# Performance work log

Measured on AMD Instinct MI355X. Metric: run time of the kernel, lower is better.

The kernel has to match this reference:

```python
import jax, jax.numpy as jnp
import numpy as np

B, S, D, H, DFF = 2, 2048, 1024, 16, 4096
DK = D // H
EPS = 1e-6


def layer_norm(x, alpha, bias):
    # torch: alpha * (x - mean) / (std_unbiased + eps) + bias
    mean = jnp.mean(x, axis=-1, keepdims=True)
    std = jnp.sqrt(jnp.var(x, axis=-1, keepdims=True, ddof=1))
    return alpha * (x - mean) / (std + EPS) + bias


def setup_inputs() -> dict:
    key = jax.random.key(0)
    ks = jax.random.split(key, 10)
    w = lambda k, shape: (jax.random.normal(k, shape, jnp.float32) * 0.02)
    return {
        "x": jax.random.normal(ks[0], (B, S, D), jnp.float32),
        "mask": jnp.ones((B, 1, 1, S), jnp.int32),
        "wq": w(ks[1], (D, D)),
        "wk": w(ks[2], (D, D)),
        "wv": w(ks[3], (D, D)),
        "wo": w(ks[4], (D, D)),
        "w1": w(ks[5], (DFF, D)),
        "b1": jnp.zeros((DFF,), jnp.float32),
        "w2": w(ks[6], (D, DFF)),
        "b2": jnp.zeros((D,), jnp.float32),
        "alpha1": jnp.ones((D,), jnp.float32),
        "bias1": jnp.zeros((D,), jnp.float32),
        "alpha2": jnp.ones((D,), jnp.float32),
        "bias2": jnp.zeros((D,), jnp.float32),
    }


def reference(x, mask, wq, wk, wv, wo, w1, b1, w2, b2, alpha1, bias1, alpha2, bias2):
    # --- residual 1: pre-norm + self-attention ---
    xn = layer_norm(x, alpha1, bias1)                      # [B,S,D]
    q = (xn @ wq.T).reshape(B, S, H, DK).transpose(0, 2, 1, 3)  # [B,H,S,DK]
    k = (xn @ wk.T).reshape(B, S, H, DK).transpose(0, 2, 1, 3)
    v = (xn @ wv.T).reshape(B, S, H, DK).transpose(0, 2, 1, 3)
    scores = jnp.einsum("bhqd,bhkd->bhqk", q, k) / jnp.sqrt(jnp.float32(DK))
    scores = jnp.where(mask == 0, jnp.float32(-1e9), scores)
    attn = jax.nn.softmax(scores, axis=-1)                 # [B,H,S,S]
    av = jnp.einsum("bhqk,bhkd->bhqd", attn, v)            # [B,H,S,DK]
    av = av.transpose(0, 2, 1, 3).reshape(B, S, D)
    x = x + av @ wo.T                                      # dropout p=0
    # --- residual 2: pre-norm + FFN ---
    xn2 = layer_norm(x, alpha2, bias2)
    h = jax.nn.relu(xn2 @ w1.T + b1)                       # [B,S,DFF]
    x = x + h @ w2.T + b2
    return x
```

## Files before the change

### kernel.cpp

```cpp
#include <hip/hip_runtime.h>

#define B_   2
#define S_   2048
#define D_   1024
#define H_   16
#define DK_  64
#define DFF_ 4096
#define NTOK (B_ * S_)

#define QSCALE 0.18033688011112042f

typedef __bf16 bf16x8 __attribute__((ext_vector_type(8)));
typedef __bf16 bf16x4 __attribute__((ext_vector_type(4)));
typedef float  f32x4  __attribute__((ext_vector_type(4)));

#if __has_builtin(__builtin_amdgcn_exp2f)
#define EXP2(x) __builtin_amdgcn_exp2f(x)
#else
#define EXP2(x) exp2f(x)
#endif

__device__ __forceinline__ void ld16(const __bf16* g, __bf16* l) {
  __builtin_amdgcn_global_load_lds(
      (const __attribute__((address_space(1))) void*)g,
      (__attribute__((address_space(3))) void*)l, 16, 0, 0);
}

#define RAW_BAR()     __asm__ __volatile__("s_barrier" ::: "memory")
#define SCHED_FENCE() __builtin_amdgcn_sched_barrier(0)

__device__ __forceinline__ void xcd_swz256(int& bx, int& by) {
  const int gx = gridDim.x;
  const int flat = blockIdx.y * gx + blockIdx.x;
  const int x = flat & 7, n = flat >> 3;
  if (gx == 16) { by = ((x >> 1) << 2) + (n >> 3); bx = ((x & 1) << 3) + (n & 7); }
  else          { by = (x << 1) + (n >> 2);        bx = n & 3; }
}

__device__ __forceinline__ void lda4(bf16x8 (&afr)[4], const __bf16* hb,
                                     int abase, int f0) {
#pragma unroll
  for (int i = 0; i < 4; ++i)
    afr[i] = *(const bf16x8*)(hb + abase + (f0 + i) * 512);
}

__device__ __forceinline__ void ldb4(bf16x8 (&bfr)[4], const __bf16* hb,
                                     int bbase) {
#pragma unroll
  for (int j = 0; j < 4; ++j)
    bfr[j] = *(const bf16x8*)(hb + bbase + j * 512);
}

__device__ __forceinline__ void mm16(f32x4 (&acc)[8][4], const bf16x8 (&afr)[4],
                                     const bf16x8 (&bfr)[4], int r0) {
#pragma unroll
  for (int i = 0; i < 4; ++i)
#pragma unroll
    for (int j = 0; j < 4; ++j)
      acc[r0 + i][j] =
          __builtin_amdgcn_mfma_f32_16x16x32_bf16(afr[i], bfr[j], acc[r0 + i][j], 0, 0, 0);
}

__device__ __forceinline__ void gemm_core_256(
    const __bf16* __restrict__ A, const __bf16* __restrict__ W,
    int ld, int kLen, int rowA0, int rowW0,
    f32x4 (&acc)[8][4], __bf16* Ls)
{
  const int t = threadIdx.x;
  const int lane = t & 63, wv = t >> 6;
  const int wm = wv >> 2, wn = wv & 3;
  const int l15 = lane & 15, q4 = lane >> 4;

  const int lane_rd = l15 * 32 + ((q4 * 8) ^ (((l15 >> 1) & 3) << 3));
  const int abase = wm * 4096 + lane_rd;
  const int bbase = wn * 2048 + lane_rd;

  const int sc0 = t ^ ((t >> 3) & 3);
  const __bf16* gA0 = A + (size_t)(rowA0 + (sc0 >> 2)) * ld + (sc0 & 3) * 8;
  const __bf16* gA1 = gA0 + (size_t)128 * ld;
  const __bf16* gW0 = W + (size_t)(rowW0 + (sc0 >> 2)) * ld + (sc0 & 3) * 8;
  const __bf16* gW1 = gW0 + (size_t)128 * ld;
  const int d0 = wv * 512, d1 = 4096 + wv * 512;

#pragma unroll
  for (int i = 0; i < 8; ++i)
#pragma unroll
    for (int j = 0; j < 4; ++j) acc[i][j] = (f32x4){0.f, 0.f, 0.f, 0.f};

#define HBASE(slot, mat, h) (Ls + ((((slot)*2) + (mat)) * 2 + (h)) * 8192)
#define STG_A(tt, h, slot) do { __bf16* _d = HBASE(slot, 0, h);              \
    const int _ko = (tt) * 64 + (h) * 32;                                    \
    ld16(gA0 + _ko, _d + d0); ld16(gA1 + _ko, _d + d1); } while (0)
#define STG_B(tt, h, slot) do { __bf16* _d = HBASE(slot, 1, h);              \
    const int _ko = (tt) * 64 + (h) * 32;                                    \
    ld16(gW0 + _ko, _d + d0); ld16(gW1 + _ko, _d + d1); } while (0)
#define MFMA_PH(r0) do { RAW_BAR(); SCHED_FENCE();                           \
    __builtin_amdgcn_s_setprio(1); mm16(acc, afr, bfr, r0);                  \
    __builtin_amdgcn_s_setprio(0); SCHED_FENCE(); RAW_BAR(); } while (0)

  const int NT = kLen >> 6;
  bf16x8 afr[4], bfr[4];

  STG_A(0, 0, 0); STG_A(0, 1, 0); STG_B(0, 0, 0); STG_B(0, 1, 0);
  STG_B(1, 0, 1); STG_A(1, 0, 1); STG_B(1, 1, 1);
  __asm__ __volatile__("s_waitcnt vmcnt(6)" ::: "memory");
  RAW_BAR(); SCHED_FENCE();

  for (int u = 0; u < NT; u += 2) {
    const bool g2 = (u + 2) < NT, g3 = (u + 3) < NT;
    lda4(afr, HBASE(0, 0, 0), abase, 0); ldb4(bfr, HBASE(0, 1, 0), bbase);
    STG_A(u + 1, 1, 1);
    MFMA_PH(0);
    lda4(afr, HBASE(0, 0, 0), abase, 4);
    if (g2) STG_B(u + 2, 0, 0);
    MFMA_PH(4);
    lda4(afr, HBASE(0, 0, 1), abase, 0); ldb4(bfr, HBASE(0, 1, 1), bbase);
    if (g2) STG_A(u + 2, 0, 0);
    MFMA_PH(0);
    lda4(afr, HBASE(0, 0, 1), abase, 4);
    if (g2) {
      STG_B(u + 2, 1, 0);
      __asm__ __volatile__("s_waitcnt vmcnt(6)" ::: "memory");
    } else {
      __asm__ __volatile__("s_waitcnt vmcnt(0)" ::: "memory");
    }
    MFMA_PH(4);
    lda4(afr, HBASE(1, 0, 0), abase, 0); ldb4(bfr, HBASE(1, 1, 0), bbase);
    if (g2) STG_A(u + 2, 1, 0);
    MFMA_PH(0);
    lda4(afr, HBASE(1, 0, 0), abase, 4);
    if (g3) STG_B(u + 3, 0, 1);
    MFMA_PH(4);
    lda4(afr, HBASE(1, 0, 1), abase, 0); ldb4(bfr, HBASE(1, 1, 1), bbase);
    if (g3) STG_A(u + 3, 0, 1);
    MFMA_PH(0);
    lda4(afr, HBASE(1, 0, 1), abase, 4);
    if (g3) STG_B(u + 3, 1, 1);
    __asm__ __volatile__("s_waitcnt vmcnt(6)" ::: "memory");
    MFMA_PH(4);
  }
#undef HBASE
#undef STG_A
#undef STG_B
#undef MFMA_PH
}

__global__ __launch_bounds__(512, 2) void gemm_qkv_256(
    const __bf16* __restrict__ xn,
    const __bf16* __restrict__ wqb, const __bf16* __restrict__ wkb,
    const __bf16* __restrict__ wvb,
    __bf16* __restrict__ qo, __bf16* __restrict__ ko, __bf16* __restrict__ vto)
{
  __shared__ __align__(16) __bf16 Ls[65536];
  int bx, by; xcd_swz256(bx, by);
  const __bf16* W = blockIdx.z == 0 ? wqb : (blockIdx.z == 1 ? wkb : wvb);
  f32x4 acc[8][4];
  gemm_core_256(xn, W, D_, D_, by * 256, bx * 256, acc, Ls);

  const int t = threadIdx.x, lane = t & 63, wv = t >> 6;
  const int wm = wv >> 2, wn = wv & 3;
  const int l15 = lane & 15, q4 = lane >> 4;
  const int row0 = by * 256 + wm * 128;
  const int col0 = bx * 256 + wn * 64;

  if (blockIdx.z < 2) {
    __bf16* o = blockIdx.z == 0 ? qo : ko;
    const float sc = blockIdx.z == 0 ? QSCALE : 1.0f;
#pragma unroll
    for (int fr = 0; fr < 8; ++fr)
#pragma unroll
      for (int fc = 0; fc < 4; ++fc) {
        const int col = col0 + fc * 16 + l15;
#pragma unroll
        for (int r = 0; r < 4; ++r) {
          const int row = row0 + fr * 16 + q4 * 4 + r;
          o[(size_t)row * D_ + col] = (__bf16)(acc[fr][fc][r] * sc);
        }
      }
  } else {
#pragma unroll
    for (int fr = 0; fr < 8; ++fr)
#pragma unroll
      for (int fc = 0; fc < 4; ++fc) {
        const int tok0 = row0 + fr * 16 + q4 * 4;
        const int c    = col0 + fc * 16 + l15;
        const int b0 = tok0 >> 11, s0 = tok0 & (S_ - 1);
        const int hh = c >> 6, dd = c & (DK_ - 1);
        bf16x4 pk;
#pragma unroll
        for (int r = 0; r < 4; ++r) pk[r] = (__bf16)acc[fr][fc][r];
        *(bf16x4*)&vto[(size_t)((b0 * H_ + hh) * DK_ + dd) * S_ + s0] = pk;
      }
  }
}

__global__ __launch_bounds__(512, 2) void gemm_ffn1_256(
    const __bf16* __restrict__ A, const __bf16* __restrict__ W,
    __bf16* __restrict__ outb, const float* __restrict__ bias)
{
  __shared__ __align__(16) __bf16 Ls[65536];
  int bx, by; xcd_swz256(bx, by);
  f32x4 acc[8][4];
  gemm_core_256(A, W, D_, D_, by * 256, bx * 256, acc, Ls);

  const int t = threadIdx.x, lane = t & 63, wv = t >> 6;
  const int wm = wv >> 2, wn = wv & 3;
  const int l15 = lane & 15, q4 = lane >> 4;
  const int row0 = by * 256 + wm * 128;
  const int col0 = bx * 256 + wn * 64;

#pragma unroll
  for (int fr = 0; fr < 8; ++fr)
#pragma unroll
    for (int fc = 0; fc < 4; ++fc) {
      const int col = col0 + fc * 16 + l15;
      const float bs = bias[col];
#pragma unroll
      for (int r = 0; r < 4; ++r) {
        const int row = row0 + fr * 16 + q4 * 4 + r;
        outb[(size_t)row * DFF_ + col] = (__bf16)fmaxf(acc[fr][fc][r] + bs, 0.0f);
      }
    }
}

__global__ __launch_bounds__(512, 2) void gemm_ffn2_sk4(
    const __bf16* __restrict__ A, const __bf16* __restrict__ W,
    __bf16* __restrict__ pp)
{
  __shared__ __align__(16) __bf16 Ls[65536];
  int bx, by; xcd_swz256(bx, by);
  const int z = blockIdx.z;
  f32x4 acc[8][4];
  gemm_core_256(A + (size_t)z * 1024, W + (size_t)z * 1024, DFF_, 1024,
                by * 256, bx * 256, acc, Ls);

  const int t = threadIdx.x, lane = t & 63, wv = t >> 6;
  const int wm = wv >> 2, wn = wv & 3;
  const int l15 = lane & 15, q4 = lane >> 4;
  const int row0 = by * 256 + wm * 128;
  const int col0 = bx * 256 + wn * 64;
  __bf16* out = pp + (size_t)z * NTOK * D_;

#pragma unroll
  for (int fr = 0; fr < 8; ++fr)
#pragma unroll
    for (int fc = 0; fc < 4; ++fc) {
      const int col = col0 + fc * 16 + l15;
#pragma unroll
      for (int r = 0; r < 4; ++r) {
        const int row = row0 + fr * 16 + q4 * 4 + r;
        out[(size_t)row * D_ + col] = (__bf16)acc[fr][fc][r];
      }
    }
}

__global__ __launch_bounds__(512, 2) void gemm_oproj_256(
    const __bf16* __restrict__ A, const __bf16* __restrict__ W,
    float* __restrict__ p0, float* __restrict__ p1)
{
  __shared__ __align__(16) __bf16 Ls[65536];
  int bx, by; xcd_swz256(bx, by);
  const int z = blockIdx.z;
  f32x4 acc[8][4];
  gemm_core_256(A + (size_t)z * 512, W + (size_t)z * 512, D_, 512,
                by * 256, bx * 256, acc, Ls);

  const int t = threadIdx.x, lane = t & 63, wv = t >> 6;
  const int wm = wv >> 2, wn = wv & 3;
  const int l15 = lane & 15, q4 = lane >> 4;
  const int row0 = by * 256 + wm * 128;
  const int col0 = bx * 256 + wn * 64;
  float* out = z == 0 ? p0 : p1;

#pragma unroll
  for (int fr = 0; fr < 8; ++fr)
#pragma unroll
    for (int fc = 0; fc < 4; ++fc) {
      const int col = col0 + fc * 16 + l15;
#pragma unroll
      for (int r = 0; r < 4; ++r) {
        const int row = row0 + fr * 16 + q4 * 4 + r;
        out[(size_t)row * D_ + col] = acc[fr][fc][r];
      }
    }
}

__global__ __launch_bounds__(256) void oproj_ln_reduce(
    const float* __restrict__ x, const float* __restrict__ p0,
    const float* __restrict__ p1, const float* __restrict__ alpha,
    const float* __restrict__ bias, float* __restrict__ x1,
    __bf16* __restrict__ xn2)
{
  const int row = blockIdx.x;
  const int t = threadIdx.x;
  const size_t base = (size_t)row * D_;
  float4 v  = ((const float4*)(x  + base))[t];
  const float4 a0 = ((const float4*)(p0 + base))[t];
  const float4 a1 = ((const float4*)(p1 + base))[t];
  v.x += a0.x + a1.x; v.y += a0.y + a1.y;
  v.z += a0.z + a1.z; v.w += a0.w + a1.w;
  ((float4*)(x1 + base))[t] = v;

  float s  = v.x + v.y + v.z + v.w;
  float ss = v.x * v.x + v.y * v.y + v.z * v.z + v.w * v.w;
#pragma unroll
  for (int m = 1; m < 64; m <<= 1) {
    s  += __shfl_xor(s, m);
    ss += __shfl_xor(ss, m);
  }
  __shared__ float red[8];
  if ((t & 63) == 0) { red[t >> 6] = s; red[4 + (t >> 6)] = ss; }
  __syncthreads();
  s  = red[0] + red[1] + red[2] + red[3];
  ss = red[4] + red[5] + red[6] + red[7];
  const float mean = s * (1.0f / D_);
  float var = (ss - (float)D_ * mean * mean) * (1.0f / (D_ - 1));
  var = fmaxf(var, 0.0f);
  const float inv = 1.0f / (sqrtf(var) + 1e-6f);
  const float4 al = ((const float4*)alpha)[t];
  const float4 bi = ((const float4*)bias)[t];
  bf16x4 o;
  o.x = (__bf16)(al.x * (v.x - mean) * inv + bi.x);
  o.y = (__bf16)(al.y * (v.y - mean) * inv + bi.y);
  o.z = (__bf16)(al.z * (v.z - mean) * inv + bi.z);
  o.w = (__bf16)(al.w * (v.w - mean) * inv + bi.w);
  ((bf16x4*)(xn2 + base))[t] = o;
}

__global__ __launch_bounds__(256) void ffn2_reduce(
    const float* __restrict__ x1, const __bf16* __restrict__ pp,
    const float* __restrict__ b2, float* __restrict__ out)
{
  const int idx4 = blockIdx.x * 256 + threadIdx.x;
  float4 v = ((const float4*)x1)[idx4];
  const float4 bs = ((const float4*)b2)[idx4 & 255];
  const size_t st = (size_t)NTOK * D_ / 4;
  const bf16x4 q0 = ((const bf16x4*)pp)[idx4];
  const bf16x4 q1 = ((const bf16x4*)pp)[idx4 + st];
  const bf16x4 q2 = ((const bf16x4*)pp)[idx4 + 2 * st];
  const bf16x4 q3 = ((const bf16x4*)pp)[idx4 + 3 * st];
  v.x += bs.x + (float)q0[0] + (float)q1[0] + (float)q2[0] + (float)q3[0];
  v.y += bs.y + (float)q0[1] + (float)q1[1] + (float)q2[1] + (float)q3[1];
  v.z += bs.z + (float)q0[2] + (float)q1[2] + (float)q2[2] + (float)q3[2];
  v.w += bs.w + (float)q0[3] + (float)q1[3] + (float)q2[3] + (float)q3[3];
  ((float4*)out)[idx4] = v;
}

struct CastJobs {
  const float* src[6];
  __bf16* dst[6];
  int n4[6];
};

__global__ __launch_bounds__(256) void cast_ln_kernel(
    CastJobs cj, const float* __restrict__ x, const float* __restrict__ alpha,
    const float* __restrict__ bias, __bf16* __restrict__ xn1)
{
  const int j = blockIdx.y;
  if (j < 6) {
    const int i = blockIdx.x * 256 + threadIdx.x;
    if (i < cj.n4[j]) {
      float4 v = ((const float4*)cj.src[j])[i];
      bf16x4 o;
      o.x = (__bf16)v.x; o.y = (__bf16)v.y; o.z = (__bf16)v.z; o.w = (__bf16)v.w;
      ((bf16x4*)cj.dst[j])[i] = o;
    }
    return;
  }
  const int row = blockIdx.x;
  const int t = threadIdx.x;
  const float4 v = ((const float4*)(x + (size_t)row * D_))[t];
  float s  = v.x + v.y + v.z + v.w;
  float ss = v.x * v.x + v.y * v.y + v.z * v.z + v.w * v.w;
#pragma unroll
  for (int m = 1; m < 64; m <<= 1) {
    s  += __shfl_xor(s, m);
    ss += __shfl_xor(ss, m);
  }
  __shared__ float red[8];
  if ((t & 63) == 0) { red[t >> 6] = s; red[4 + (t >> 6)] = ss; }
  __syncthreads();
  s  = red[0] + red[1] + red[2] + red[3];
  ss = red[4] + red[5] + red[6] + red[7];
  const float mean = s * (1.0f / D_);
  float var = (ss - (float)D_ * mean * mean) * (1.0f / (D_ - 1));
  var = fmaxf(var, 0.0f);
  const float inv = 1.0f / (sqrtf(var) + 1e-6f);
  const float4 al = ((const float4*)alpha)[t];
  const float4 bi = ((const float4*)bias)[t];
  bf16x4 o;
  o.x = (__bf16)(al.x * (v.x - mean) * inv + bi.x);
  o.y = (__bf16)(al.y * (v.y - mean) * inv + bi.y);
  o.z = (__bf16)(al.z * (v.z - mean) * inv + bi.z);
  o.w = (__bf16)(al.w * (v.w - mean) * inv + bi.w);
  ((bf16x4*)(xn1 + (size_t)row * D_))[t] = o;
}

__global__ __launch_bounds__(256) void attn_kernel(
    const __bf16* __restrict__ qg, const __bf16* __restrict__ kg,
    const __bf16* __restrict__ vtg, const int* __restrict__ mask,
    __bf16* __restrict__ av)
{
  __shared__ __align__(16) __bf16 Ks[2][64 * 64];
  __shared__ __align__(16) __bf16 Vt[2][64 * 64];
  __shared__ __align__(16) __bf16 Ps[128 * 72];
  __shared__ int Dd[32];

  const int t = threadIdx.x, lane = t & 63, wv = t >> 6;
  const int l15 = lane & 15, q4 = lane >> 4;
  const int bh = blockIdx.x;
  const int b = bh >> 4, h = bh & (H_ - 1);
  const int q0 = blockIdx.y * 128;

  const int srow = lane & 7, sc8 = lane >> 3;
  const __bf16* qg0 = qg + (size_t)(b * S_ + q0 + 32 * wv + srow) * D_ + h * DK_ + sc8 * 8;
  __bf16* lQ = Ps + wv * 2304;
#pragma unroll
  for (int p = 0; p < 4; ++p)
    ld16(qg0 + (size_t)(8 * p) * D_, lQ + 512 * p);

  const __bf16* kg0 = kg + (size_t)(b * S_ + 16 * wv + srow) * D_ + h * DK_ + sc8 * 8;
  const __bf16* vt0 = vtg + (size_t)(bh * DK_ + 16 * wv + srow) * S_ + sc8 * 8;

  if (t < 32) Dd[t] = 0;

  ld16(kg0,                  Ks[0] + wv * 1024);
  ld16(kg0 + (size_t)8 * D_, Ks[0] + wv * 1024 + 512);
  ld16(vt0,                  Vt[0] + wv * 1024);
  ld16(vt0 + (size_t)8 * S_, Vt[0] + wv * 1024 + 512);

  __syncthreads();

  {
    const int4* m4 = (const int4*)(mask + (size_t)b * S_) + t * 2;
    const int4 a = m4[0], c = m4[1];
    const bool anyz = (a.x == 0) | (a.y == 0) | (a.z == 0) | (a.w == 0) |
                      (c.x == 0) | (c.y == 0) | (c.z == 0) | (c.w == 0);
    if (anyz) Dd[t >> 3] = 1;
  }
  __syncthreads();
  const bool blockDirty = (__ballot(Dd[lane & 31] != 0) != 0ull);

  const int fb = ((l15 >> 3) << 9) + (q4 << 6) + ((l15 & 7) << 3);
  const int mrow = b * S_;

  bf16x8 bq[2][2];
#pragma unroll
  for (int j = 0; j < 2; ++j)
#pragma unroll
    for (int s = 0; s < 2; ++s)
      bq[j][s] = *(const bf16x8*)(lQ + j * 1024 + s * 256 + fb);

  bf16x8 bones;
#pragma unroll
  for (int e = 0; e < 8; ++e) bones[e] = (__bf16)1.0f;

  f32x4 lacc[2];
  f32x4 oacc[2][4];
#pragma unroll
  for (int m = 0; m < 2; ++m) {
    lacc[m] = (f32x4){0.f, 0.f, 0.f, 0.f};
#pragma unroll
    for (int jd = 0; jd < 4; ++jd) oacc[m][jd] = (f32x4){0.f, 0.f, 0.f, 0.f};
  }

  for (int kv0 = 0; kv0 < S_; kv0 += 64) {
    const int buf = (kv0 >> 6) & 1;
    if (kv0 + 64 < S_) {
      const size_t nk = (size_t)(kv0 + 64);
      ld16(kg0 + nk * D_,              Ks[buf ^ 1] + wv * 1024);
      ld16(kg0 + (nk + 8) * D_,        Ks[buf ^ 1] + wv * 1024 + 512);
      ld16(vt0 + nk,                   Vt[buf ^ 1] + wv * 1024);
      ld16(vt0 + (size_t)8 * S_ + nk,  Vt[buf ^ 1] + wv * 1024 + 512);
    }

    f32x4 sacc[4][2];
#pragma unroll
    for (int i = 0; i < 4; ++i)
#pragma unroll
      for (int j = 0; j < 2; ++j) sacc[i][j] = (f32x4){0.f, 0.f, 0.f, 0.f};
    __builtin_amdgcn_s_setprio(1);
#pragma unroll
    for (int i = 0; i < 4; ++i)
#pragma unroll
      for (int s = 0; s < 2; ++s) {
        bf16x8 ak = *(const bf16x8*)(Ks[buf] + i * 1024 + fb + s * 256);
#pragma unroll
        for (int j = 0; j < 2; ++j)
          sacc[i][j] = __builtin_amdgcn_mfma_f32_16x16x32_bf16(ak, bq[j][s], sacc[i][j], 0, 0, 0);
      }
    __builtin_amdgcn_s_setprio(0);

    if (blockDirty && Dd[kv0 >> 6]) {
#pragma unroll
      for (int i = 0; i < 4; ++i)
#pragma unroll
        for (int r = 0; r < 4; ++r)
          if (mask[mrow + kv0 + 16 * i + 4 * q4 + r] == 0) {
            sacc[i][0][r] = -1e30f;
            sacc[i][1][r] = -1e30f;
          }
    }

#pragma unroll
    for (int j = 0; j < 2; ++j)
#pragma unroll
      for (int i = 0; i < 4; ++i) {
        bf16x4 pb;
#pragma unroll
        for (int r = 0; r < 4; ++r) pb[r] = (__bf16)EXP2(sacc[i][j][r]);
        *(bf16x4*)(Ps + (wv * 32 + j * 16 + l15) * 72 + 16 * i + q4 * 4) = pb;
      }

    bf16x8 ap[2][2];
#pragma unroll
    for (int m = 0; m < 2; ++m)
#pragma unroll
      for (int s = 0; s < 2; ++s)
        ap[m][s] = *(const bf16x8*)(Ps + (wv * 32 + 16 * m + l15) * 72 + s * 32 + q4 * 8);
    __builtin_amdgcn_s_setprio(1);
#pragma unroll
    for (int jd = 0; jd < 4; ++jd)
#pragma unroll
      for (int s = 0; s < 2; ++s) {
        bf16x8 bv = *(const bf16x8*)(Vt[buf] + jd * 1024 + fb + s * 256);
#pragma unroll
        for (int m = 0; m < 2; ++m)
          oacc[m][jd] = __builtin_amdgcn_mfma_f32_16x16x32_bf16(ap[m][s], bv, oacc[m][jd], 0, 0, 0);
      }
#pragma unroll
    for (int m = 0; m < 2; ++m)
#pragma unroll
      for (int s = 0; s < 2; ++s)
        lacc[m] = __builtin_amdgcn_mfma_f32_16x16x32_bf16(ap[m][s], bones, lacc[m], 0, 0, 0);
    __builtin_amdgcn_s_setprio(0);

    __syncthreads();
  }

#pragma unroll
  for (int m = 0; m < 2; ++m) {
    f32x4 lt;
#pragma unroll
    for (int r = 0; r < 4; ++r) lt[r] = 1.0f / lacc[m][r];
#pragma unroll
    for (int jd = 0; jd < 4; ++jd)
#pragma unroll
      for (int r = 0; r < 4; ++r) {
        int tok = b * S_ + q0 + wv * 32 + 16 * m + q4 * 4 + r;
        int c   = h * DK_ + jd * 16 + l15;
        av[(size_t)tok * D_ + c] = (__bf16)(oacc[m][jd][r] * lt[r]);
      }
  }
}

extern "C" void kernel_launch(void* const* d_in, const int* in_sizes, int n_in,
                              void* d_out, int out_size, void* d_ws, size_t ws_size,
                              hipStream_t stream) {
  const float* x      = (const float*)d_in[0];
  const int*   mask   = (const int*)d_in[1];
  const float* wq     = (const float*)d_in[2];
  const float* wk     = (const float*)d_in[3];
  const float* wv     = (const float*)d_in[4];
  const float* wo     = (const float*)d_in[5];
  const float* w1     = (const float*)d_in[6];
  const float* b1     = (const float*)d_in[7];
  const float* w2     = (const float*)d_in[8];
  const float* b2     = (const float*)d_in[9];
  const float* alpha1 = (const float*)d_in[10];
  const float* bias1  = (const float*)d_in[11];
  const float* alpha2 = (const float*)d_in[12];
  const float* bias2  = (const float*)d_in[13];

  char* ws = (char*)d_ws;
  __bf16* wqb = (__bf16*)(ws + ((size_t)0 << 20));
  __bf16* wkb = (__bf16*)(ws + ((size_t)2 << 20));
  __bf16* wvb = (__bf16*)(ws + ((size_t)4 << 20));
  __bf16* wob = (__bf16*)(ws + ((size_t)6 << 20));
  __bf16* w1b = (__bf16*)(ws + ((size_t)8 << 20));
  __bf16* w2b = (__bf16*)(ws + ((size_t)16 << 20));
  __bf16* xn1 = (__bf16*)(ws + ((size_t)24 << 20));
  __bf16* qb  = (__bf16*)(ws + ((size_t)32 << 20));
  __bf16* kb  = (__bf16*)(ws + ((size_t)40 << 20));
  __bf16* vtb = (__bf16*)(ws + ((size_t)48 << 20));
  __bf16* avb = (__bf16*)(ws + ((size_t)56 << 20));
  float*  x1  = (float*) (ws + ((size_t)64 << 20));
  __bf16* xn2 = (__bf16*)(ws + ((size_t)56 << 20));
  __bf16* hb  = (__bf16*)(ws + ((size_t)24 << 20));
  float*  op0 = (float*) (ws + ((size_t)24 << 20));
  float*  op1 = (float*) (ws + ((size_t)40 << 20));
  __bf16* fpp = (__bf16*)(ws + ((size_t)32 << 20));

  CastJobs cj;
  cj.src[0] = wq; cj.dst[0] = wqb; cj.n4[0] = D_ * D_ / 4;
  cj.src[1] = wk; cj.dst[1] = wkb; cj.n4[1] = D_ * D_ / 4;
  cj.src[2] = wv; cj.dst[2] = wvb; cj.n4[2] = D_ * D_ / 4;
  cj.src[3] = wo; cj.dst[3] = wob; cj.n4[3] = D_ * D_ / 4;
  cj.src[4] = w1; cj.dst[4] = w1b; cj.n4[4] = DFF_ * D_ / 4;
  cj.src[5] = w2; cj.dst[5] = w2b; cj.n4[5] = DFF_ * D_ / 4;

  cast_ln_kernel<<<dim3(DFF_ * D_ / 4 / 256, 7), 256, 0, stream>>>(
      cj, x, alpha1, bias1, xn1);

  gemm_qkv_256<<<dim3(D_ / 256, NTOK / 256, 3), 512, 0, stream>>>(
      xn1, wqb, wkb, wvb, qb, kb, vtb);

  attn_kernel<<<dim3(B_ * H_, S_ / 128), 256, 0, stream>>>(qb, kb, vtb, mask, avb);

  gemm_oproj_256<<<dim3(D_ / 256, NTOK / 256, 2), 512, 0, stream>>>(
      avb, wob, op0, op1);

  oproj_ln_reduce<<<dim3(NTOK), 256, 0, stream>>>(
      x, op0, op1, alpha2, bias2, x1, xn2);

  gemm_ffn1_256<<<dim3(DFF_ / 256, NTOK / 256), 512, 0, stream>>>(
      xn2, w1b, hb, b1);

  gemm_ffn2_sk4<<<dim3(D_ / 256, NTOK / 256, 4), 512, 0, stream>>>(
      hb, w2b, fpp);

  ffn2_reduce<<<dim3(NTOK * D_ / 4 / 256), 256, 0, stream>>>(
      x1, fpp, b2, (float*)d_out);
}
```

Measured before the change: 332.6 us.

## Split-K4 bf16 o-proj partials, register P permute in attention, fold residual into output

The output projection now splits K four ways and writes bf16 partials in place of two fp32 partials, which halves reduce traffic. The LN reduce kernel writes x1+b2 straight into the output buffer, so the separate x1 buffer and its re-read are gone. ffn2_reduce then accumulates the four FFN2 partials in place into that buffer. In attention, softmax probabilities are rearranged with permlane swaps in registers instead of a round trip through LDS, and the score MFMA chain starts from zero. The cost is more o-proj blocks with shorter K, extra bf16 rounding of the partials, and dependence on permlane swap builtins or a ds_swizzle fallback.

```diff
diff --git a/kernel.cpp b/kernel.cpp
--- a/kernel.cpp
+++ b/kernel.cpp
@@ -12,7 +12,9 @@
 
 typedef __bf16 bf16x8 __attribute__((ext_vector_type(8)));
 typedef __bf16 bf16x4 __attribute__((ext_vector_type(4)));
+typedef __bf16 bf16x2 __attribute__((ext_vector_type(2)));
 typedef float  f32x4  __attribute__((ext_vector_type(4)));
+typedef int    i32x4  __attribute__((ext_vector_type(4)));
 
 #if __has_builtin(__builtin_amdgcn_exp2f)
 #define EXP2(x) __builtin_amdgcn_exp2f(x)
@@ -28,6 +30,37 @@
 
 #define RAW_BAR()     __asm__ __volatile__("s_barrier" ::: "memory")
 #define SCHED_FENCE() __builtin_amdgcn_sched_barrier(0)
+
+__device__ __forceinline__ int packbf(float lo, float hi) {
+  bf16x2 r; r[0] = (__bf16)lo; r[1] = (__bf16)hi;
+  return __builtin_bit_cast(int, r);
+}
+
+__device__ __forceinline__ void swap32(int a, int b, int& g0, int& g1, bool hi32) {
+#if __has_builtin(__builtin_amdgcn_permlane32_swap)
+  auto r = __builtin_amdgcn_permlane32_swap(a, b, false, false);
+  g0 = r[0]; g1 = r[1];
+  (void)hi32;
+#else
+  const int sa = __builtin_amdgcn_ds_swizzle(a, 0x801F);
+  const int sb = __builtin_amdgcn_ds_swizzle(b, 0x801F);
+  g0 = hi32 ? sb : a;
+  g1 = hi32 ? b : sa;
+#endif
+}
+
+__device__ __forceinline__ void swap16(int a, int b, int& h0, int& h1, bool hi16) {
+#if __has_builtin(__builtin_amdgcn_permlane16_swap)
+  auto r = __builtin_amdgcn_permlane16_swap(a, b, false, false);
+  h0 = r[0]; h1 = r[1];
+  (void)hi16;
+#else
+  const int sa = __builtin_amdgcn_ds_swizzle(a, 0x401F);
+  const int sb = __builtin_amdgcn_ds_swizzle(b, 0x401F);
+  h0 = hi16 ? sb : a;
+  h1 = hi16 ? b : sa;
+#endif
+}
 
 __device__ __forceinline__ void xcd_swz256(int& bx, int& by) {
   const int gx = gridDim.x;
@@ -225,7 +258,8 @@
 
 __global__ __launch_bounds__(512, 2) void gemm_ffn2_sk4(
     const __bf16* __restrict__ A, const __bf16* __restrict__ W,
-    __bf16* __restrict__ pp)
+    __bf16* __restrict__ p0, __bf16* __restrict__ p1,
+    __bf16* __restrict__ p2, __bf16* __restrict__ p3)
 {
   __shared__ __align__(16) __bf16 Ls[65536];
   int bx, by; xcd_swz256(bx, by);
@@ -239,7 +273,7 @@
   const int l15 = lane & 15, q4 = lane >> 4;
   const int row0 = by * 256 + wm * 128;
   const int col0 = bx * 256 + wn * 64;
-  __bf16* out = pp + (size_t)z * NTOK * D_;
+  __bf16* out = z == 0 ? p0 : (z == 1 ? p1 : (z == 2 ? p2 : p3));
 
 #pragma unroll
   for (int fr = 0; fr < 8; ++fr)
@@ -254,15 +288,15 @@
     }
 }
 
-__global__ __launch_bounds__(512, 2) void gemm_oproj_256(
+__global__ __launch_bounds__(512, 2) void gemm_oproj_sk4(
     const __bf16* __restrict__ A, const __bf16* __restrict__ W,
-    float* __restrict__ p0, float* __restrict__ p1)
+    __bf16* __restrict__ pp)
 {
   __shared__ __align__(16) __bf16 Ls[65536];
   int bx, by; xcd_swz256(bx, by);
   const int z = blockIdx.z;
   f32x4 acc[8][4];
-  gemm_core_256(A + (size_t)z * 512, W + (size_t)z * 512, D_, 512,
+  gemm_core_256(A + (size_t)z * 256, W + (size_t)z * 256, D_, 256,
                 by * 256, bx * 256, acc, Ls);
 
   const int t = threadIdx.x, lane = t & 63, wv = t >> 6;
@@ -270,7 +304,7 @@
   const int l15 = lane & 15, q4 = lane >> 4;
   const int row0 = by * 256 + wm * 128;
   const int col0 = bx * 256 + wn * 64;
-  float* out = z == 0 ? p0 : p1;
+  __bf16* out = pp + (size_t)z * NTOK * D_;
 
 #pragma unroll
   for (int fr = 0; fr < 8; ++fr)
@@ -280,26 +314,36 @@
 #pragma unroll
       for (int r = 0; r < 4; ++r) {
         const int row = row0 + fr * 16 + q4 * 4 + r;
-        out[(size_t)row * D_ + col] = acc[fr][fc][r];
+        out[(size_t)row * D_ + col] = (__bf16)acc[fr][fc][r];
       }
     }
 }
 
 __global__ __launch_bounds__(256) void oproj_ln_reduce(
-    const float* __restrict__ x, const float* __restrict__ p0,
-    const float* __restrict__ p1, const float* __restrict__ alpha,
-    const float* __restrict__ bias, float* __restrict__ x1,
+    const float* __restrict__ x, const __bf16* __restrict__ opp,
+    const float* __restrict__ alpha, const float* __restrict__ bias,
+    const float* __restrict__ b2, float* __restrict__ dout,
     __bf16* __restrict__ xn2)
 {
   const int row = blockIdx.x;
   const int t = threadIdx.x;
   const size_t base = (size_t)row * D_;
-  float4 v  = ((const float4*)(x  + base))[t];
-  const float4 a0 = ((const float4*)(p0 + base))[t];
-  const float4 a1 = ((const float4*)(p1 + base))[t];
-  v.x += a0.x + a1.x; v.y += a0.y + a1.y;
-  v.z += a0.z + a1.z; v.w += a0.w + a1.w;
-  ((float4*)(x1 + base))[t] = v;
+  const size_t st4 = (size_t)NTOK * D_ / 4;
+  const size_t i4 = base / 4 + t;
+  float4 v = ((const float4*)(x + base))[t];
+  const bf16x4 a0 = ((const bf16x4*)opp)[i4];
+  const bf16x4 a1 = ((const bf16x4*)opp)[i4 + st4];
+  const bf16x4 a2 = ((const bf16x4*)opp)[i4 + 2 * st4];
+  const bf16x4 a3 = ((const bf16x4*)opp)[i4 + 3 * st4];
+  v.x += (float)a0[0] + (float)a1[0] + (float)a2[0] + (float)a3[0];
+  v.y += (float)a0[1] + (float)a1[1] + (float)a2[1] + (float)a3[1];
+  v.z += (float)a0[2] + (float)a1[2] + (float)a2[2] + (float)a3[2];
+  v.w += (float)a0[3] + (float)a1[3] + (float)a2[3] + (float)a3[3];
+
+  const float4 bb = ((const float4*)b2)[t];
+  float4 o4;
+  o4.x = v.x + bb.x; o4.y = v.y + bb.y; o4.z = v.z + bb.z; o4.w = v.w + bb.w;
+  ((float4*)(dout + base))[t] = o4;
 
   float s  = v.x + v.y + v.z + v.w;
   float ss = v.x * v.x + v.y * v.y + v.z * v.z + v.w * v.w;
@@ -328,21 +372,20 @@
 }
 
 __global__ __launch_bounds__(256) void ffn2_reduce(
-    const float* __restrict__ x1, const __bf16* __restrict__ pp,
-    const float* __restrict__ b2, float* __restrict__ out)
+    const __bf16* __restrict__ p0, const __bf16* __restrict__ p1,
+    const __bf16* __restrict__ p2, const __bf16* __restrict__ p3,
+    float* __restrict__ out)
 {
   const int idx4 = blockIdx.x * 256 + threadIdx.x;
-  float4 v = ((const float4*)x1)[idx4];
-  const float4 bs = ((const float4*)b2)[idx4 & 255];
-  const size_t st = (size_t)NTOK * D_ / 4;
-  const bf16x4 q0 = ((const bf16x4*)pp)[idx4];
-  const bf16x4 q1 = ((const bf16x4*)pp)[idx4 + st];
-  const bf16x4 q2 = ((const bf16x4*)pp)[idx4 + 2 * st];
-  const bf16x4 q3 = ((const bf16x4*)pp)[idx4 + 3 * st];
-  v.x += bs.x + (float)q0[0] + (float)q1[0] + (float)q2[0] + (float)q3[0];
-  v.y += bs.y + (float)q0[1] + (float)q1[1] + (float)q2[1] + (float)q3[1];
-  v.z += bs.z + (float)q0[2] + (float)q1[2] + (float)q2[2] + (float)q3[2];
-  v.w += bs.w + (float)q0[3] + (float)q1[3] + (float)q2[3] + (float)q3[3];
+  float4 v = ((const float4*)out)[idx4];
+  const bf16x4 q0 = ((const bf16x4*)p0)[idx4];
+  const bf16x4 q1 = ((const bf16x4*)p1)[idx4];
+  const bf16x4 q2 = ((const bf16x4*)p2)[idx4];
+  const bf16x4 q3 = ((const bf16x4*)p3)[idx4];
+  v.x += (float)q0[0] + (float)q1[0] + (float)q2[0] + (float)q3[0];
+  v.y += (float)q0[1] + (float)q1[1] + (float)q2[1] + (float)q3[1];
+  v.z += (float)q0[2] + (float)q1[2] + (float)q2[2] + (float)q3[2];
+  v.w += (float)q0[3] + (float)q1[3] + (float)q2[3] + (float)q3[3];
   ((float4*)out)[idx4] = v;
 }
 
@@ -401,20 +444,21 @@
     const __bf16* __restrict__ vtg, const int* __restrict__ mask,
     __bf16* __restrict__ av)
 {
-  __shared__ __align__(16) __bf16 Ks[2][64 * 64];
-  __shared__ __align__(16) __bf16 Vt[2][64 * 64];
-  __shared__ __align__(16) __bf16 Ps[128 * 72];
+  __shared__ __align__(16) __bf16 Ks[2][4096];
+  __shared__ __align__(16) __bf16 Vt[2][4096];
+  __shared__ __align__(16) __bf16 Qs[8192];
   __shared__ int Dd[32];
 
   const int t = threadIdx.x, lane = t & 63, wv = t >> 6;
   const int l15 = lane & 15, q4 = lane >> 4;
+  const bool hi16 = (lane & 16) != 0, hi32 = (lane & 32) != 0;
   const int bh = blockIdx.x;
   const int b = bh >> 4, h = bh & (H_ - 1);
   const int q0 = blockIdx.y * 128;
 
   const int srow = lane & 7, sc8 = lane >> 3;
   const __bf16* qg0 = qg + (size_t)(b * S_ + q0 + 32 * wv + srow) * D_ + h * DK_ + sc8 * 8;
-  __bf16* lQ = Ps + wv * 2304;
+  __bf16* lQ = Qs + wv * 2048;
 #pragma unroll
   for (int p = 0; p < 4; ++p)
     ld16(qg0 + (size_t)(8 * p) * D_, lQ + 512 * p);
@@ -454,14 +498,15 @@
   bf16x8 bones;
 #pragma unroll
   for (int e = 0; e < 8; ++e) bones[e] = (__bf16)1.0f;
+  const f32x4 z4 = {0.f, 0.f, 0.f, 0.f};
 
   f32x4 lacc[2];
   f32x4 oacc[2][4];
 #pragma unroll
   for (int m = 0; m < 2; ++m) {
-    lacc[m] = (f32x4){0.f, 0.f, 0.f, 0.f};
-#pragma unroll
-    for (int jd = 0; jd < 4; ++jd) oacc[m][jd] = (f32x4){0.f, 0.f, 0.f, 0.f};
+    lacc[m] = z4;
+#pragma unroll
+    for (int jd = 0; jd < 4; ++jd) oacc[m][jd] = z4;
   }
 
   for (int kv0 = 0; kv0 < S_; kv0 += 64) {
@@ -475,20 +520,16 @@
     }
 
     f32x4 sacc[4][2];
-#pragma unroll
-    for (int i = 0; i < 4; ++i)
-#pragma unroll
-      for (int j = 0; j < 2; ++j) sacc[i][j] = (f32x4){0.f, 0.f, 0.f, 0.f};
     __builtin_amdgcn_s_setprio(1);
 #pragma unroll
-    for (int i = 0; i < 4; ++i)
-#pragma unroll
-      for (int s = 0; s < 2; ++s) {
-        bf16x8 ak = *(const bf16x8*)(Ks[buf] + i * 1024 + fb + s * 256);
-#pragma unroll
-        for (int j = 0; j < 2; ++j)
-          sacc[i][j] = __builtin_amdgcn_mfma_f32_16x16x32_bf16(ak, bq[j][s], sacc[i][j], 0, 0, 0);
-      }
+    for (int i = 0; i < 4; ++i) {
+      const bf16x8 ak0 = *(const bf16x8*)(Ks[buf] + i * 1024 + fb);
+      const bf16x8 ak1 = *(const bf16x8*)(Ks[buf] + i * 1024 + fb + 256);
+      sacc[i][0] = __builtin_amdgcn_mfma_f32_16x16x32_bf16(ak0, bq[0][0], z4, 0, 0, 0);
+      sacc[i][1] = __builtin_amdgcn_mfma_f32_16x16x32_bf16(ak0, bq[1][0], z4, 0, 0, 0);
+      sacc[i][0] = __builtin_amdgcn_mfma_f32_16x16x32_bf16(ak1, bq[0][1], sacc[i][0], 0, 0, 0);
+      sacc[i][1] = __builtin_amdgcn_mfma_f32_16x16x32_bf16(ak1, bq[1][1], sacc[i][1], 0, 0, 0);
+    }
     __builtin_amdgcn_s_setprio(0);
 
     if (blockDirty && Dd[kv0 >> 6]) {
@@ -503,21 +544,31 @@
     }
 
 #pragma unroll
+    for (int i = 0; i < 4; ++i)
+#pragma unroll
+      for (int j = 0; j < 2; ++j)
+#pragma unroll
+        for (int r = 0; r < 4; ++r)
+          sacc[i][j][r] = EXP2(sacc[i][j][r]);
+
+    bf16x8 ap[2][2];
+#pragma unroll
     for (int j = 0; j < 2; ++j)
 #pragma unroll
-      for (int i = 0; i < 4; ++i) {
-        bf16x4 pb;
-#pragma unroll
-        for (int r = 0; r < 4; ++r) pb[r] = (__bf16)EXP2(sacc[i][j][r]);
-        *(bf16x4*)(Ps + (wv * 32 + j * 16 + l15) * 72 + 16 * i + q4 * 4) = pb;
-      }
-
-    bf16x8 ap[2][2];
-#pragma unroll
-    for (int m = 0; m < 2; ++m)
-#pragma unroll
-      for (int s = 0; s < 2; ++s)
-        ap[m][s] = *(const bf16x8*)(Ps + (wv * 32 + 16 * m + l15) * 72 + s * 32 + q4 * 8);
+      for (int s = 0; s < 2; ++s) {
+        const int pa0 = packbf(sacc[2 * s][j][0],     sacc[2 * s][j][1]);
+        const int pa1 = packbf(sacc[2 * s][j][2],     sacc[2 * s][j][3]);
+        const int pb0 = packbf(sacc[2 * s + 1][j][0], sacc[2 * s + 1][j][1]);
+        const int pb1 = packbf(sacc[2 * s + 1][j][2], sacc[2 * s + 1][j][3]);
+        int g0, g1, g2, g3, h0, h1, h2, h3;
+        swap32(pa0, pb0, g0, g1, hi32);
+        swap32(pa1, pb1, g2, g3, hi32);
+        swap16(g0, g1, h0, h1, hi16);
+        swap16(g2, g3, h2, h3, hi16);
+        i32x4 fw; fw[0] = h0; fw[1] = h2; fw[2] = h1; fw[3] = h3;
+        ap[j][s] = __builtin_bit_cast(bf16x8, fw);
+      }
+
     __builtin_amdgcn_s_setprio(1);
 #pragma unroll
     for (int jd = 0; jd < 4; ++jd)
@@ -584,12 +635,13 @@
   __bf16* kb  = (__bf16*)(ws + ((size_t)40 << 20));
   __bf16* vtb = (__bf16*)(ws + ((size_t)48 << 20));
   __bf16* avb = (__bf16*)(ws + ((size_t)56 << 20));
-  float*  x1  = (float*) (ws + ((size_t)64 << 20));
+  __bf16* opp = (__bf16*)(ws + ((size_t)24 << 20));
   __bf16* xn2 = (__bf16*)(ws + ((size_t)56 << 20));
   __bf16* hb  = (__bf16*)(ws + ((size_t)24 << 20));
-  float*  op0 = (float*) (ws + ((size_t)24 << 20));
-  float*  op1 = (float*) (ws + ((size_t)40 << 20));
-  __bf16* fpp = (__bf16*)(ws + ((size_t)32 << 20));
+  __bf16* fp0 = (__bf16*)(ws + ((size_t)0 << 20));
+  __bf16* fp1 = (__bf16*)(ws + ((size_t)8 << 20));
+  __bf16* fp2 = (__bf16*)(ws + ((size_t)56 << 20));
+  __bf16* fp3 = (__bf16*)(ws + ((size_t)64 << 20));
 
   CastJobs cj;
   cj.src[0] = wq; cj.dst[0] = wqb; cj.n4[0] = D_ * D_ / 4;
@@ -607,18 +659,18 @@
 
   attn_kernel<<<dim3(B_ * H_, S_ / 128), 256, 0, stream>>>(qb, kb, vtb, mask, avb);
 
-  gemm_oproj_256<<<dim3(D_ / 256, NTOK / 256, 2), 512, 0, stream>>>(
-      avb, wob, op0, op1);
+  gemm_oproj_sk4<<<dim3(D_ / 256, NTOK / 256, 4), 512, 0, stream>>>(
+      avb, wob, opp);
 
   oproj_ln_reduce<<<dim3(NTOK), 256, 0, stream>>>(
-      x, op0, op1, alpha2, bias2, x1, xn2);
+      x, opp, alpha2, bias2, b2, (float*)d_out, xn2);
 
   gemm_ffn1_256<<<dim3(DFF_ / 256, NTOK / 256), 512, 0, stream>>>(
       xn2, w1b, hb, b1);
 
   gemm_ffn2_sk4<<<dim3(D_ / 256, NTOK / 256, 4), 512, 0, stream>>>(
-      hb, w2b, fpp);
+      hb, w2b, fp0, fp1, fp2, fp3);
 
   ffn2_reduce<<<dim3(NTOK * D_ / 4 / 256), 256, 0, stream>>>(
-      x1, fpp, b2, (float*)d_out);
-}
+      fp0, fp1, fp2, fp3, (float*)d_out);
+}
```

Result: faster. 322.6 us (-3.0%).
